# Kernel optimization log

Hardware: AMD Instinct MI355X
Metric: run time of the kernel (lower is better)

## Reference

```python
import jax, jax.numpy as jnp
import numpy as np

ALPHA = 0.2  # LeakyReLU negative slope


def setup_inputs() -> dict:
    key = jax.random.key(0)
    k1, k2, k3 = jax.random.split(key, 3)
    B, N, IN, OUT = 64, 2048, 1024, 1024
    features = jax.random.normal(k1, (B, N, IN), dtype=jnp.float32)
    # Xavier-uniform-ish scaling for weights
    W = jax.random.normal(k2, (OUT, IN), dtype=jnp.float32) * (1.0 / np.sqrt(IN))
    w_b = jnp.zeros((OUT,), dtype=jnp.float32)
    a_w = jax.random.normal(k3, (2 * OUT,), dtype=jnp.float32) * (1.0 / np.sqrt(2 * OUT))
    a_b = jnp.zeros((), dtype=jnp.float32)
    bias_out = jnp.zeros((OUT,), dtype=jnp.float32)
    return {"features": features, "W": W, "w_b": w_b, "a_w": a_w, "a_b": a_b, "bias_out": bias_out}


def reference(features, W, w_b, a_w, a_b, bias_out):
    # h = Linear(in_dim, out_dim)(features): [B, N, D]
    h = jnp.einsum('bni,di->bnd', features, W) + w_b
    D = h.shape[-1]
    a1, a2 = a_w[:D], a_w[D:]
    # concat([h_expand, h]) @ a == h[:, :1] . a1 + h . a2  (h_expand broadcasts node 0)
    e = (h[:, 0:1, :] @ a1[:, None]) + jnp.einsum('bnd,d->bn', h, a2)[..., None] + a_b  # [B, N, 1]
    e = jnp.where(e >= 0, e, ALPHA * e)  # LeakyReLU
    attention = jax.nn.softmax(e, axis=1)  # softmax over nodes, [B, N, 1]
    # dropout p=0.0 -> identity
    pooled = jnp.einsum('bnk,bnd->bkd', attention, h)  # [B, 1, D]
    return jax.nn.relu(pooled + bias_out)
```

## Files before the change

kernel.cpp:

```cpp
#include <hip/hip_runtime.h>

#define ALPHA 0.2f
constexpr int B_   = 64;
constexpr int N_   = 2048;
constexpr int IN_  = 1024;
constexpr int OUT_ = 1024;
constexpr int CHUNK = 256;
constexpr int NCH   = N_ / CHUNK;
constexpr int RPW   = CHUNK / 4;

constexpr size_t WA1   = 0;
constexpr size_t WA2   = 1024;
constexpr size_t C12   = 2048;
constexpr size_t E0    = 2112;
constexpr size_t ZPART = 2176;
constexpr size_t GPART = 4096;
constexpr size_t GV    = GPART + (size_t)B_ * NCH * IN_;

__device__ inline float wave_reduce_sum(float v) {
    #pragma unroll
    for (int off = 32; off > 0; off >>= 1) v += __shfl_xor(v, off);
    return v;
}

__global__ void kA(const float* __restrict__ W, const float* __restrict__ aw,
                   float* __restrict__ ws) {
    int t   = threadIdx.x;
    int col = blockIdx.x * 64 + (t & 63);
    int dg  = t >> 6;
    const float* a1 = aw;
    const float* a2 = aw + OUT_;
    float acc1 = 0.f, acc2 = 0.f;
    for (int d = dg * 256; d < dg * 256 + 256; ++d) {
        float w = W[(size_t)d * IN_ + col];
        acc1 += w * a1[d];
        acc2 += w * a2[d];
    }
    __shared__ float r1[4][64], r2[4][64];
    r1[dg][t & 63] = acc1;
    r2[dg][t & 63] = acc2;
    __syncthreads();
    if (t < 64) {
        ws[WA1 + blockIdx.x * 64 + t] = r1[0][t] + r1[1][t] + r1[2][t] + r1[3][t];
        ws[WA2 + blockIdx.x * 64 + t] = r2[0][t] + r2[1][t] + r2[2][t] + r2[3][t];
    }
}

__global__ void kG(const float* __restrict__ wb, const float* __restrict__ aw,
                   float* __restrict__ ws) {
    int t = threadIdx.x;
    float p1 = 0.f, p2 = 0.f;
    for (int d = t; d < OUT_; d += 256) {
        p1 += wb[d] * aw[d];
        p2 += wb[d] * aw[OUT_ + d];
    }
    __shared__ float r1[256], r2[256];
    r1[t] = p1; r2[t] = p2;
    __syncthreads();
    for (int off = 128; off > 0; off >>= 1) {
        if (t < off) { r1[t] += r1[t + off]; r2[t] += r2[t + off]; }
        __syncthreads();
    }
    if (t == 0) { ws[C12] = r1[0]; ws[C12 + 1] = r2[0]; }
}

__global__ void kP(const float* __restrict__ f, float* __restrict__ ws) {
    int t = threadIdx.x, wave = t >> 6, lane = t & 63;
    int b = blockIdx.x * 4 + wave;
    const float4* f4    = (const float4*)(f + (size_t)b * N_ * IN_);
    const float4* wa1_4 = (const float4*)(ws + WA1);
    float a = 0.f;
    #pragma unroll
    for (int k = 0; k < 4; ++k) {
        float4 v  = f4[k * 64 + lane];
        float4 w1 = wa1_4[k * 64 + lane];
        a += v.x * w1.x + v.y * w1.y + v.z * w1.z + v.w * w1.w;
    }
    a = wave_reduce_sum(a);
    if (lane == 0) ws[E0 + b] = a;
}

__global__ void kMain(const float* __restrict__ f, const float* __restrict__ ab,
                      float* __restrict__ ws) {
    int b = blockIdx.y, chunk = blockIdx.x;
    int t = threadIdx.x, wave = t >> 6, lane = t & 63;
    float cst = ws[E0 + b] + ws[C12] + ws[C12 + 1] + ab[0];

    const float4* wa2_4 = (const float4*)(ws + WA2);
    float4 ra2[4];
    #pragma unroll
    for (int k = 0; k < 4; ++k) ra2[k] = wa2_4[k * 64 + lane];

    const float4* fbase = (const float4*)(f + ((size_t)b * N_ + (size_t)chunk * CHUNK) * IN_);
    float4 acc[4];
    #pragma unroll
    for (int k = 0; k < 4; ++k) acc[k] = make_float4(0.f, 0.f, 0.f, 0.f);
    float z = 0.f;

    float4 v[4], nv[4];
    int r = wave;
    #pragma unroll
    for (int k = 0; k < 4; ++k) v[k] = fbase[(size_t)r * 256 + k * 64 + lane];

    for (int i = 0; i < RPW; ++i) {
        int rn = r + 4;
        if (i + 1 < RPW) {
            #pragma unroll
            for (int k = 0; k < 4; ++k) nv[k] = fbase[(size_t)rn * 256 + k * 64 + lane];
        }
        float dot = 0.f;
        #pragma unroll
        for (int k = 0; k < 4; ++k)
            dot += v[k].x * ra2[k].x + v[k].y * ra2[k].y + v[k].z * ra2[k].z + v[k].w * ra2[k].w;
        dot = wave_reduce_sum(dot);
        float e = dot + cst;
        e = e >= 0.f ? e : ALPHA * e;
        float w = __expf(e);
        z += w;
        #pragma unroll
        for (int k = 0; k < 4; ++k) {
            acc[k].x += w * v[k].x; acc[k].y += w * v[k].y;
            acc[k].z += w * v[k].z; acc[k].w += w * v[k].w;
        }
        if (i + 1 < RPW) {
            #pragma unroll
            for (int k = 0; k < 4; ++k) v[k] = nv[k];
        }
        r = rn;
    }

    __shared__ float4 gbuf[4][256];
    __shared__ float  zbuf[4];
    #pragma unroll
    for (int k = 0; k < 4; ++k) gbuf[wave][k * 64 + lane] = acc[k];
    if (lane == 0) zbuf[wave] = z;
    __syncthreads();
    float4 s0 = gbuf[0][t], s1 = gbuf[1][t], s2 = gbuf[2][t], s3 = gbuf[3][t];
    float4 s = make_float4(s0.x + s1.x + s2.x + s3.x, s0.y + s1.y + s2.y + s3.y,
                           s0.z + s1.z + s2.z + s3.z, s0.w + s1.w + s2.w + s3.w);
    ((float4*)(ws + GPART))[((size_t)b * NCH + chunk) * 256 + t] = s;
    if (t == 0) ws[ZPART + b * NCH + chunk] = zbuf[0] + zbuf[1] + zbuf[2] + zbuf[3];
}

__global__ void kE(float* __restrict__ ws) {
    int b = blockIdx.x, t = threadIdx.x;
    __shared__ float zinv;
    if (t == 0) {
        float zz = 0.f;
        #pragma unroll
        for (int c = 0; c < NCH; ++c) zz += ws[ZPART + b * NCH + c];
        zinv = 1.0f / zz;
    }
    __syncthreads();
    const float4* gp = (const float4*)(ws + GPART);
    float4 acc = make_float4(0.f, 0.f, 0.f, 0.f);
    #pragma unroll
    for (int c = 0; c < NCH; ++c) {
        float4 v = gp[((size_t)b * NCH + c) * 256 + t];
        acc.x += v.x; acc.y += v.y; acc.z += v.z; acc.w += v.w;
    }
    acc.x *= zinv; acc.y *= zinv; acc.z *= zinv; acc.w *= zinv;
    ((float4*)(ws + GV))[b * 256 + t] = acc;
}

__global__ void kF(const float* __restrict__ W, const float* __restrict__ wb,
                   const float* __restrict__ bias, const float* __restrict__ ws,
                   float* __restrict__ out) {
    int b = blockIdx.x, t = threadIdx.x;
    int dbase = blockIdx.y * 4;
    __shared__ float sg[IN_];
    ((float4*)sg)[t] = ((const float4*)(ws + GV))[b * 256 + t];
    __syncthreads();
    int wave = t >> 6, lane = t & 63;
    int d = dbase + wave;
    const float4* w4 = (const float4*)(W + (size_t)d * IN_);
    float acc = 0.f;
    #pragma unroll
    for (int k = 0; k < 4; ++k) {
        float4 wv = w4[k * 64 + lane];
        int i = (k * 64 + lane) * 4;
        acc += wv.x * sg[i] + wv.y * sg[i + 1] + wv.z * sg[i + 2] + wv.w * sg[i + 3];
    }
    acc = wave_reduce_sum(acc);
    if (lane == 0) {
        float p = acc + wb[d] + bias[d];
        out[(size_t)b * OUT_ + d] = p > 0.f ? p : 0.f;
    }
}

extern "C" void kernel_launch(void* const* d_in, const int* in_sizes, int n_in,
                              void* d_out, int out_size, void* d_ws, size_t ws_size,
                              hipStream_t stream) {
    const float* f    = (const float*)d_in[0];
    const float* W    = (const float*)d_in[1];
    const float* wb   = (const float*)d_in[2];
    const float* aw   = (const float*)d_in[3];
    const float* ab   = (const float*)d_in[4];
    const float* bias = (const float*)d_in[5];
    float* out = (float*)d_out;
    float* ws  = (float*)d_ws;

    kA<<<dim3(IN_ / 64), 256, 0, stream>>>(W, aw, ws);
    kG<<<dim3(1), 256, 0, stream>>>(wb, aw, ws);
    kP<<<dim3(B_ / 4), 256, 0, stream>>>(f, ws);
    kMain<<<dim3(NCH, B_), 256, 0, stream>>>(f, ab, ws);
    kE<<<dim3(B_), 256, 0, stream>>>(ws);
    kF<<<dim3(B_, OUT_ / 4), 256, 0, stream>>>(W, wb, bias, ws, out);
}
```

Measured before the change: 135.0 us.

## Split W·a projection into parallel partials, halve chunk size, restructure final GEMV

Measured after the change: 148.8 us. 10.2% more time.

```diff
diff --git a/kernel.cpp b/kernel.cpp
--- a/kernel.cpp
+++ b/kernel.cpp
@@ -5,17 +5,18 @@
 constexpr int N_   = 2048;
 constexpr int IN_  = 1024;
 constexpr int OUT_ = 1024;
-constexpr int CHUNK = 256;
+constexpr int CHUNK = 128;
 constexpr int NCH   = N_ / CHUNK;
 constexpr int RPW   = CHUNK / 4;
 
 constexpr size_t WA1   = 0;
 constexpr size_t WA2   = 1024;
-constexpr size_t C12   = 2048;
-constexpr size_t E0    = 2112;
-constexpr size_t ZPART = 2176;
-constexpr size_t GPART = 4096;
-constexpr size_t GV    = GPART + (size_t)B_ * NCH * IN_;
+constexpr size_t E0    = 2048;
+constexpr size_t ZPART = 2112;
+constexpr size_t PART1 = 4096;
+constexpr size_t PART2 = 135168;
+constexpr size_t GPART = 270336;
+constexpr size_t GV    = 1318912;
 
 __device__ inline float wave_reduce_sum(float v) {
     #pragma unroll
@@ -23,68 +24,59 @@
     return v;
 }
 
-__global__ void kA(const float* __restrict__ W, const float* __restrict__ aw,
-                   float* __restrict__ ws) {
-    int t   = threadIdx.x;
-    int col = blockIdx.x * 64 + (t & 63);
-    int dg  = t >> 6;
-    const float* a1 = aw;
-    const float* a2 = aw + OUT_;
-    float acc1 = 0.f, acc2 = 0.f;
-    for (int d = dg * 256; d < dg * 256 + 256; ++d) {
-        float w = W[(size_t)d * IN_ + col];
-        acc1 += w * a1[d];
-        acc2 += w * a2[d];
-    }
-    __shared__ float r1[4][64], r2[4][64];
-    r1[dg][t & 63] = acc1;
-    r2[dg][t & 63] = acc2;
-    __syncthreads();
-    if (t < 64) {
-        ws[WA1 + blockIdx.x * 64 + t] = r1[0][t] + r1[1][t] + r1[2][t] + r1[3][t];
-        ws[WA2 + blockIdx.x * 64 + t] = r2[0][t] + r2[1][t] + r2[2][t] + r2[3][t];
-    }
-}
-
-__global__ void kG(const float* __restrict__ wb, const float* __restrict__ aw,
-                   float* __restrict__ ws) {
-    int t = threadIdx.x;
-    float p1 = 0.f, p2 = 0.f;
-    for (int d = t; d < OUT_; d += 256) {
-        p1 += wb[d] * aw[d];
-        p2 += wb[d] * aw[OUT_ + d];
-    }
-    __shared__ float r1[256], r2[256];
-    r1[t] = p1; r2[t] = p2;
+__global__ void kA1(const float* __restrict__ W, const float* __restrict__ aw,
+                    float* __restrict__ ws) {
+    int t = threadIdx.x, blk = blockIdx.x;
+    float4 acc1 = make_float4(0.f, 0.f, 0.f, 0.f);
+    float4 acc2 = make_float4(0.f, 0.f, 0.f, 0.f);
+    #pragma unroll
+    for (int r = 0; r < 8; ++r) {
+        int d = blk * 8 + r;
+        float a1 = aw[d], a2 = aw[OUT_ + d];
+        float4 w = ((const float4*)(W + (size_t)d * IN_))[t];
+        acc1.x += a1 * w.x; acc1.y += a1 * w.y; acc1.z += a1 * w.z; acc1.w += a1 * w.w;
+        acc2.x += a2 * w.x; acc2.y += a2 * w.y; acc2.z += a2 * w.z; acc2.w += a2 * w.w;
+    }
+    ((float4*)(ws + PART1))[blk * 256 + t] = acc1;
+    ((float4*)(ws + PART2))[blk * 256 + t] = acc2;
+}
+
+__global__ void kA2(float* __restrict__ ws) {
+    int idx = blockIdx.x * 256 + threadIdx.x;
+    int which = idx >> 10, col = idx & 1023;
+    const float* p = ws + (which ? PART2 : PART1) + col;
+    float s = 0.f;
+    #pragma unroll 8
+    for (int r = 0; r < 128; ++r) s += p[(size_t)r * 1024];
+    ws[(which ? WA2 : WA1) + col] = s;
+}
+
+__global__ void kP(const float* __restrict__ f, const float* __restrict__ wb,
+                   const float* __restrict__ aw, float* __restrict__ ws) {
+    int b = blockIdx.x, t = threadIdx.x;
+    float4 v   = ((const float4*)(f + (size_t)b * N_ * IN_))[t];
+    float4 w1  = ((const float4*)(ws + WA1))[t];
+    float4 wbv = ((const float4*)wb)[t];
+    float4 a1v = ((const float4*)aw)[t];
+    float4 a2v = ((const float4*)(aw + OUT_))[t];
+    float p = v.x * w1.x + v.y * w1.y + v.z * w1.z + v.w * w1.w
+            + wbv.x * (a1v.x + a2v.x) + wbv.y * (a1v.y + a2v.y)
+            + wbv.z * (a1v.z + a2v.z) + wbv.w * (a1v.w + a2v.w);
+    __shared__ float red[256];
+    red[t] = p;
     __syncthreads();
     for (int off = 128; off > 0; off >>= 1) {
-        if (t < off) { r1[t] += r1[t + off]; r2[t] += r2[t + off]; }
+        if (t < off) red[t] += red[t + off];
         __syncthreads();
     }
-    if (t == 0) { ws[C12] = r1[0]; ws[C12 + 1] = r2[0]; }
-}
-
-__global__ void kP(const float* __restrict__ f, float* __restrict__ ws) {
-    int t = threadIdx.x, wave = t >> 6, lane = t & 63;
-    int b = blockIdx.x * 4 + wave;
-    const float4* f4    = (const float4*)(f + (size_t)b * N_ * IN_);
-    const float4* wa1_4 = (const float4*)(ws + WA1);
-    float a = 0.f;
-    #pragma unroll
-    for (int k = 0; k < 4; ++k) {
-        float4 v  = f4[k * 64 + lane];
-        float4 w1 = wa1_4[k * 64 + lane];
-        a += v.x * w1.x + v.y * w1.y + v.z * w1.z + v.w * w1.w;
-    }
-    a = wave_reduce_sum(a);
-    if (lane == 0) ws[E0 + b] = a;
+    if (t == 0) ws[E0 + b] = red[0];
 }
 
 __global__ void kMain(const float* __restrict__ f, const float* __restrict__ ab,
                       float* __restrict__ ws) {
     int b = blockIdx.y, chunk = blockIdx.x;
     int t = threadIdx.x, wave = t >> 6, lane = t & 63;
-    float cst = ws[E0 + b] + ws[C12] + ws[C12 + 1] + ab[0];
+    float cst = ws[E0 + b] + ab[0];
 
     const float4* wa2_4 = (const float4*)(ws + WA2);
     float4 ra2[4];
@@ -166,25 +158,27 @@
 __global__ void kF(const float* __restrict__ W, const float* __restrict__ wb,
                    const float* __restrict__ bias, const float* __restrict__ ws,
                    float* __restrict__ out) {
-    int b = blockIdx.x, t = threadIdx.x;
-    int dbase = blockIdx.y * 4;
-    __shared__ float sg[IN_];
-    ((float4*)sg)[t] = ((const float4*)(ws + GV))[b * 256 + t];
-    __syncthreads();
-    int wave = t >> 6, lane = t & 63;
-    int d = dbase + wave;
+    int t = threadIdx.x, wave = t >> 6, lane = t & 63;
+    int d = blockIdx.x * 4 + wave;
     const float4* w4 = (const float4*)(W + (size_t)d * IN_);
-    float acc = 0.f;
-    #pragma unroll
-    for (int k = 0; k < 4; ++k) {
-        float4 wv = w4[k * 64 + lane];
-        int i = (k * 64 + lane) * 4;
-        acc += wv.x * sg[i] + wv.y * sg[i + 1] + wv.z * sg[i + 2] + wv.w * sg[i + 3];
-    }
-    acc = wave_reduce_sum(acc);
-    if (lane == 0) {
-        float p = acc + wb[d] + bias[d];
-        out[(size_t)b * OUT_ + d] = p > 0.f ? p : 0.f;
+    float4 wreg[4];
+    #pragma unroll
+    for (int k = 0; k < 4; ++k) wreg[k] = w4[k * 64 + lane];
+    float wbb = wb[d] + bias[d];
+    const float4* gv = (const float4*)(ws + GV);
+    #pragma unroll 4
+    for (int b = 0; b < B_; ++b) {
+        float acc = 0.f;
+        #pragma unroll
+        for (int k = 0; k < 4; ++k) {
+            float4 g = gv[b * 256 + k * 64 + lane];
+            acc += g.x * wreg[k].x + g.y * wreg[k].y + g.z * wreg[k].z + g.w * wreg[k].w;
+        }
+        acc = wave_reduce_sum(acc);
+        if (lane == 0) {
+            float p = acc + wbb;
+            out[(size_t)b * OUT_ + d] = p > 0.f ? p : 0.f;
+        }
     }
 }
 
@@ -200,10 +194,10 @@
     float* out = (float*)d_out;
     float* ws  = (float*)d_ws;
 
-    kA<<<dim3(IN_ / 64), 256, 0, stream>>>(W, aw, ws);
-    kG<<<dim3(1), 256, 0, stream>>>(wb, aw, ws);
-    kP<<<dim3(B_ / 4), 256, 0, stream>>>(f, ws);
+    kA1<<<dim3(128), 256, 0, stream>>>(W, aw, ws);
+    kA2<<<dim3(8), 256, 0, stream>>>(ws);
+    kP <<<dim3(B_), 256, 0, stream>>>(f, wb, aw, ws);
     kMain<<<dim3(NCH, B_), 256, 0, stream>>>(f, ab, ws);
-    kE<<<dim3(B_), 256, 0, stream>>>(ws);
-    kF<<<dim3(B_, OUT_ / 4), 256, 0, stream>>>(W, wb, bias, ws, out);
-}
+    kE <<<dim3(B_), 256, 0, stream>>>(ws);
+    kF <<<dim3(OUT_ / 4), 256, 0, stream>>>(W, wb, bias, ws, out);
+}
```
